# Kernel tuning notes

Hardware: AMD Instinct MI355X
Metric: run time of the kernel (lower is better)

Reference implementation:

```python
import jax, jax.numpy as jnp
import numpy as np

B, L, R, E, D = 16, 28, 64, 34, 512


def setup_inputs() -> dict:
    key = jax.random.key(0)
    ks = jax.random.split(key, 10)
    logits = jax.random.uniform(ks[0], (B, L, R), dtype=jnp.float32)
    evt_embeddings = jax.random.normal(ks[1], (B, 1, D), dtype=jnp.float32)
    arg_embeddings = jax.random.normal(ks[2], (B, L, D), dtype=jnp.float32)
    # valid-arg counts in [1, L] (used as mask-count multiplier and divisor)
    arg_padding_num = jax.random.randint(ks[3], (B,), 1, L + 1).astype(jnp.float32)
    evt_type_list = jax.random.randint(ks[4], (B,), 0, E)
    s = 1.0 / np.sqrt(D)
    WRT = jax.random.normal(ks[5], (R, D, D), dtype=jnp.float32) * s
    WTT = jax.random.normal(ks[6], (E, D, D), dtype=jnp.float32) * s
    w1 = jax.random.normal(ks[7], (D, 64), dtype=jnp.float32) * s
    b1 = jnp.zeros((64,), dtype=jnp.float32)
    w2 = jax.random.normal(ks[8], (64, 1), dtype=jnp.float32) * (1.0 / 8.0)
    b2 = jnp.zeros((1,), dtype=jnp.float32)
    return {"logits": logits, "evt_embeddings": evt_embeddings,
            "arg_embeddings": arg_embeddings, "arg_padding_num": arg_padding_num,
            "evt_type_list": evt_type_list, "WRT": WRT, "WTT": WTT,
            "w1": w1, "b1": b1, "w2": w2, "b2": b2}


def reference(logits, evt_embeddings, arg_embeddings, arg_padding_num,
              evt_type_list, WRT, WTT, w1, b1, w2, b2):
    # role transition matrix per (event, arg): one-hot/soft select over WRT
    # [B,L,R] x [R,D,D] -> [B,L,D,D]  (dominant, memory-bound intermediate)
    role_mats = jnp.einsum('blr,rde->blde', logits, WRT)
    # event transition matrix: one-hot select over WTT == gather
    evt_mats = WTT[evt_type_list]                      # [B,D,D]
    # event embedding transform: [B,1,D] bmm [B,D,D] -> [B,D]
    evt_trans = jnp.einsum('bd,bde->be', evt_embeddings[:, 0, :], evt_mats)
    # per-arg transform: [B,L,D] bmm [B,L,D,D] -> [B,L,D]
    role_trans = jnp.einsum('bld,blde->ble', arg_embeddings, role_mats)
    # multiply by count, sum over args, divide by count (as in the original)
    role_trans = role_trans * arg_padding_num[:, None, None]
    new_sum = jnp.sum(role_trans, axis=1)              # [B,D]
    div = new_sum / arg_padding_num[:, None]
    graph_embeddings = (div + evt_trans) / 2.0         # [B,D]
    # scorer MLP: Linear(D,64) -> ReLU -> Linear(64,1) -> Sigmoid
    h = jax.nn.relu(graph_embeddings @ w1 + b1)
    score = jax.nn.sigmoid(h @ w2 + b2)                # [B,1]
    return score
```

## Files before the change

kernel.cpp:

```cpp
#include <hip/hip_runtime.h>
#include <math.h>

#define BB 16
#define LL 28
#define RR 64
#define DD 512
#define NROLE 256
#define NEVT  256

__global__ void __launch_bounds__(256, 2) kernel_a(
    const float* __restrict__ logits,
    const float* __restrict__ arg,
    const float* __restrict__ WRT,
    const float* __restrict__ WTT,
    const float* __restrict__ evt_emb,
    const int*   __restrict__ evt_type,
    float* __restrict__ part,
    float* __restrict__ evt_part)
{
    __shared__ float smem[8192];
    const int t   = threadIdx.x;
    const int bid = blockIdx.x;

    if (bid < NROLE) {
        const int rid = bid;
        const int rp  = rid >> 3;
        const int d0  = (rid & 7) * 64;

        const float4* Wp0 = (const float4*)(WRT + ((size_t)(2 * rp)     * DD + d0) * DD);
        const float4* Wp1 = (const float4*)(WRT + ((size_t)(2 * rp + 1) * DD + d0) * DD);

        const int e4    = t & 127;
        const int h     = t >> 7;
        const int kbase = 32 * h;

        float4 w[8];
#pragma unroll
        for (int i = 0; i < 8; ++i)
            w[i] = Wp0[(size_t)(kbase + i) * 128 + e4];

        {
            const int b  = t >> 4;
            const int d4 = t & 15;
            const float4* ap = (const float4*)(arg) + (size_t)(b * LL) * 128 + (d0 >> 2) + d4;
            const float2* lp = (const float2*)(logits + (size_t)(b * LL) * RR) + rp;
            float4 g0 = {0.f, 0.f, 0.f, 0.f};
            float4 g1 = {0.f, 0.f, 0.f, 0.f};
#pragma unroll 7
            for (int l = 0; l < LL; ++l) {
                const float4 av = ap[(size_t)l * 128];
                const float2 lg = lp[(size_t)l * 32];
                g0.x = fmaf(lg.x, av.x, g0.x); g0.y = fmaf(lg.x, av.y, g0.y);
                g0.z = fmaf(lg.x, av.z, g0.z); g0.w = fmaf(lg.x, av.w, g0.w);
                g1.x = fmaf(lg.y, av.x, g1.x); g1.y = fmaf(lg.y, av.y, g1.y);
                g1.z = fmaf(lg.y, av.z, g1.z); g1.w = fmaf(lg.y, av.w, g1.w);
            }
            smem[(4 * d4 + 0) * 16 + b] = g0.x;
            smem[(4 * d4 + 1) * 16 + b] = g0.y;
            smem[(4 * d4 + 2) * 16 + b] = g0.z;
            smem[(4 * d4 + 3) * 16 + b] = g0.w;
            smem[1024 + (4 * d4 + 0) * 16 + b] = g1.x;
            smem[1024 + (4 * d4 + 1) * 16 + b] = g1.y;
            smem[1024 + (4 * d4 + 2) * 16 + b] = g1.z;
            smem[1024 + (4 * d4 + 3) * 16 + b] = g1.w;
        }
        __syncthreads();

        float4 acc[16];
#pragma unroll
        for (int i = 0; i < 16; ++i) acc[i] = make_float4(0.f, 0.f, 0.f, 0.f);

        for (int mb = 0; mb < 8; ++mb) {
            const int mbn = (mb + 1) & 7;
            const float4* Wn = (mbn & 4) ? Wp1 : Wp0;
            const int kn = kbase + (mbn & 3) * 8;
            float4 wn[8];
#pragma unroll
            for (int i = 0; i < 8; ++i)
                wn[i] = Wn[(size_t)(kn + i) * 128 + e4];

            const float* Gr = smem + (mb & 4) * 256;
            const int k0 = kbase + (mb & 3) * 8;
#pragma unroll
            for (int i = 0; i < 8; ++i) {
                const float* gp = Gr + (k0 + i) * 16;
                const float4 ga = ((const float4*)gp)[0];
                const float4 gb = ((const float4*)gp)[1];
                const float4 gc = ((const float4*)gp)[2];
                const float4 gd = ((const float4*)gp)[3];
#define ACC(j, S) \
                acc[j].x = fmaf(S, w[i].x, acc[j].x); \
                acc[j].y = fmaf(S, w[i].y, acc[j].y); \
                acc[j].z = fmaf(S, w[i].z, acc[j].z); \
                acc[j].w = fmaf(S, w[i].w, acc[j].w);
                ACC(0,  ga.x) ACC(1,  ga.y) ACC(2,  ga.z) ACC(3,  ga.w)
                ACC(4,  gb.x) ACC(5,  gb.y) ACC(6,  gb.z) ACC(7,  gb.w)
                ACC(8,  gc.x) ACC(9,  gc.y) ACC(10, gc.z) ACC(11, gc.w)
                ACC(12, gd.x) ACC(13, gd.y) ACC(14, gd.z) ACC(15, gd.w)
#undef ACC
            }
#pragma unroll
            for (int i = 0; i < 8; ++i) w[i] = wn[i];
        }

        __syncthreads();
        float4* cb = (float4*)smem;
        if (h == 1) {
#pragma unroll
            for (int i = 0; i < 16; ++i)
                cb[i * 128 + e4] = acc[i];
        }
        __syncthreads();
        if (h == 0) {
            float4* po = (float4*)part + (size_t)rid * 2048;
#pragma unroll
            for (int i = 0; i < 16; ++i) {
                const float4 v = cb[i * 128 + e4];
                acc[i].x += v.x; acc[i].y += v.y; acc[i].z += v.z; acc[i].w += v.w;
                po[i * 128 + e4] = acc[i];
            }
        }
    } else {
        const int cid = bid - NROLE;
        const int b   = cid >> 4;
        const int dc  = cid & 15;
        const int d0  = dc * 32;
        const int ty  = evt_type[b];
        const float* Wt = WTT + (size_t)ty * DD * DD;
        const int e4 = t & 127;
        const int s  = t >> 7;
        float4 a = {0.f, 0.f, 0.f, 0.f};
#pragma unroll
        for (int db = 0; db < 32; db += 16) {
            float  em[8];
            float4 wv[8];
#pragma unroll
            for (int i = 0; i < 8; ++i) {
                const int d = d0 + db + s + 2 * i;
                em[i] = evt_emb[b * DD + d];
                wv[i] = ((const float4*)(Wt + (size_t)d * DD))[e4];
            }
#pragma unroll
            for (int i = 0; i < 8; ++i) {
                a.x = fmaf(em[i], wv[i].x, a.x);
                a.y = fmaf(em[i], wv[i].y, a.y);
                a.z = fmaf(em[i], wv[i].z, a.z);
                a.w = fmaf(em[i], wv[i].w, a.w);
            }
        }
        float4* sm4 = (float4*)smem;
        if (s == 1) sm4[e4] = a;
        __syncthreads();
        if (s == 0) {
            const float4 q4 = sm4[e4];
            a.x += q4.x; a.y += q4.y; a.z += q4.z; a.w += q4.w;
            ((float4*)evt_part)[(size_t)cid * 128 + e4] = a;
        }
    }
}

__global__ void __launch_bounds__(256) kernel_reduce(
    const float* __restrict__ part,
    const float* __restrict__ evt_part,
    float* __restrict__ div_acc,
    float* __restrict__ evt_acc)
{
    const int t = threadIdx.x;
    if (blockIdx.x < 128) {
        __shared__ float4 sred[256];
        const int oo = t & 15;
        const int pg = t >> 4;
        const int o4 = blockIdx.x * 16 + oo;
        const float4* p4 = (const float4*)part;
        float4 s = {0.f, 0.f, 0.f, 0.f};
#pragma unroll 8
        for (int i = 0; i < 16; ++i) {
            const int p = pg * 16 + i;
            const float4 v = p4[(size_t)p * 2048 + o4];
            s.x += v.x; s.y += v.y; s.z += v.z; s.w += v.w;
        }
        sred[pg * 16 + oo] = s;
        __syncthreads();
        if (t < 16) {
            float4 tot = sred[t];
#pragma unroll
            for (int g = 1; g < 16; ++g) {
                const float4 v = sred[g * 16 + t];
                tot.x += v.x; tot.y += v.y; tot.z += v.z; tot.w += v.w;
            }
            ((float4*)div_acc)[blockIdx.x * 16 + t] = tot;
        }
    } else {
        const int o4 = (blockIdx.x - 128) * 256 + t;
        const int b  = o4 >> 7;
        const int el = o4 & 127;
        const float4* e4p = (const float4*)evt_part;
        float4 s = {0.f, 0.f, 0.f, 0.f};
#pragma unroll
        for (int dc = 0; dc < 16; ++dc) {
            const float4 v = e4p[(size_t)(b * 16 + dc) * 128 + el];
            s.x += v.x; s.y += v.y; s.z += v.z; s.w += v.w;
        }
        ((float4*)evt_acc)[o4] = s;
    }
}

__global__ void __launch_bounds__(256) kernel_mlp(
    const float* __restrict__ div_acc,
    const float* __restrict__ evt_acc,
    const float* __restrict__ w1,
    const float* __restrict__ b1,
    const float* __restrict__ w2,
    const float* __restrict__ b2,
    float* __restrict__ out)
{
    __shared__ float hred[256];
    const int b  = blockIdx.x;
    const int t  = threadIdx.x;
    const int j  = t & 63;
    const int dq = t >> 6;
    float hp = 0.f;
#pragma unroll 8
    for (int i = 0; i < 128; ++i) {
        const int d = dq * 128 + i;
        const float g = (div_acc[b * DD + d] + evt_acc[b * DD + d]) * 0.5f;
        hp = fmaf(g, w1[d * 64 + j], hp);
    }
    hred[t] = hp;
    __syncthreads();
    if (t < 64) {
        float h = b1[j] + hred[j] + hred[64 + j] + hred[128 + j] + hred[192 + j];
        h = fmaxf(h, 0.f);
        float v = h * w2[j];
#pragma unroll
        for (int off = 32; off > 0; off >>= 1) v += __shfl_down(v, off, 64);
        if (j == 0) out[b] = 1.f / (1.f + expf(-(v + b2[0])));
    }
}

extern "C" void kernel_launch(void* const* d_in, const int* in_sizes, int n_in,
                              void* d_out, int out_size, void* d_ws, size_t ws_size,
                              hipStream_t stream) {
    const float* logits   = (const float*)d_in[0];
    const float* evt_emb  = (const float*)d_in[1];
    const float* arg_emb  = (const float*)d_in[2];
    const int*   evt_type = (const int*)d_in[4];
    const float* WRT      = (const float*)d_in[5];
    const float* WTT      = (const float*)d_in[6];
    const float* w1       = (const float*)d_in[7];
    const float* b1       = (const float*)d_in[8];
    const float* w2       = (const float*)d_in[9];
    const float* b2       = (const float*)d_in[10];
    float* out = (float*)d_out;

    float* part     = (float*)d_ws;
    float* evt_part = part + (size_t)NROLE * 8192;
    float* div_acc  = evt_part + (size_t)NEVT * DD;
    float* evt_acc  = div_acc + BB * DD;

    hipLaunchKernelGGL(kernel_a, dim3(NROLE + NEVT), dim3(256), 0, stream,
                       logits, arg_emb, WRT, WTT, evt_emb, evt_type, part, evt_part);
    hipLaunchKernelGGL(kernel_reduce, dim3(136), dim3(256), 0, stream,
                       part, evt_part, div_acc, evt_acc);
    hipLaunchKernelGGL(kernel_mlp, dim3(BB), dim3(256), 0, stream,
                       div_acc, evt_acc, w1, b1, w2, b2, out);
}
```

Measured before the change: 152.1 us.

## Process four roles per block and fuse reduction with MLP tail kernel

Each role block now folds four role matrices (instead of two) into its accumulator, which halves the number of role blocks and the partial-sum traffic written to the workspace. The separate reduce and MLP kernels are merged into a single 1024-thread-per-batch tail kernel that reduces the partials, forms the graph embedding in shared memory, and runs the scorer. This removes one launch and a global round trip. In exchange there are fewer blocks to fill the GPU during the dominant WRT streaming phase, each block runs a longer serial loop, and the tail uses only 16 blocks.

```diff
diff --git a/kernel.cpp b/kernel.cpp
--- a/kernel.cpp
+++ b/kernel.cpp
@@ -5,8 +5,9 @@
 #define LL 28
 #define RR 64
 #define DD 512
-#define NROLE 256
+#define NROLE 128
 #define NEVT  256
+#define F4RR  65536
 
 __global__ void __launch_bounds__(256, 2) kernel_a(
     const float* __restrict__ logits,
@@ -27,8 +28,7 @@
         const int rp  = rid >> 3;
         const int d0  = (rid & 7) * 64;
 
-        const float4* Wp0 = (const float4*)(WRT + ((size_t)(2 * rp)     * DD + d0) * DD);
-        const float4* Wp1 = (const float4*)(WRT + ((size_t)(2 * rp + 1) * DD + d0) * DD);
+        const float4* WBase = (const float4*)(WRT + ((size_t)(4 * rp) * DD + d0) * DD);
 
         const int e4    = t & 127;
         const int h     = t >> 7;
@@ -37,32 +37,45 @@
         float4 w[8];
 #pragma unroll
         for (int i = 0; i < 8; ++i)
-            w[i] = Wp0[(size_t)(kbase + i) * 128 + e4];
+            w[i] = WBase[(size_t)(kbase + i) * 128 + e4];
 
         {
             const int b  = t >> 4;
             const int d4 = t & 15;
             const float4* ap = (const float4*)(arg) + (size_t)(b * LL) * 128 + (d0 >> 2) + d4;
-            const float2* lp = (const float2*)(logits + (size_t)(b * LL) * RR) + rp;
-            float4 g0 = {0.f, 0.f, 0.f, 0.f};
-            float4 g1 = {0.f, 0.f, 0.f, 0.f};
+            const float4* lp = (const float4*)(logits) + (size_t)(b * LL) * 16 + rp;
+            float4 g0 = {0.f,0.f,0.f,0.f}, g1 = {0.f,0.f,0.f,0.f};
+            float4 g2 = {0.f,0.f,0.f,0.f}, g3 = {0.f,0.f,0.f,0.f};
 #pragma unroll 7
             for (int l = 0; l < LL; ++l) {
                 const float4 av = ap[(size_t)l * 128];
-                const float2 lg = lp[(size_t)l * 32];
+                const float4 lg = lp[(size_t)l * 16];
                 g0.x = fmaf(lg.x, av.x, g0.x); g0.y = fmaf(lg.x, av.y, g0.y);
                 g0.z = fmaf(lg.x, av.z, g0.z); g0.w = fmaf(lg.x, av.w, g0.w);
                 g1.x = fmaf(lg.y, av.x, g1.x); g1.y = fmaf(lg.y, av.y, g1.y);
                 g1.z = fmaf(lg.y, av.z, g1.z); g1.w = fmaf(lg.y, av.w, g1.w);
-            }
-            smem[(4 * d4 + 0) * 16 + b] = g0.x;
-            smem[(4 * d4 + 1) * 16 + b] = g0.y;
-            smem[(4 * d4 + 2) * 16 + b] = g0.z;
-            smem[(4 * d4 + 3) * 16 + b] = g0.w;
-            smem[1024 + (4 * d4 + 0) * 16 + b] = g1.x;
-            smem[1024 + (4 * d4 + 1) * 16 + b] = g1.y;
-            smem[1024 + (4 * d4 + 2) * 16 + b] = g1.z;
-            smem[1024 + (4 * d4 + 3) * 16 + b] = g1.w;
+                g2.x = fmaf(lg.z, av.x, g2.x); g2.y = fmaf(lg.z, av.y, g2.y);
+                g2.z = fmaf(lg.z, av.z, g2.z); g2.w = fmaf(lg.z, av.w, g2.w);
+                g3.x = fmaf(lg.w, av.x, g3.x); g3.y = fmaf(lg.w, av.y, g3.y);
+                g3.z = fmaf(lg.w, av.z, g3.z); g3.w = fmaf(lg.w, av.w, g3.w);
+            }
+            const int row = 4 * d4;
+            smem[       (row + 0) * 16 + b] = g0.x;
+            smem[       (row + 1) * 16 + b] = g0.y;
+            smem[       (row + 2) * 16 + b] = g0.z;
+            smem[       (row + 3) * 16 + b] = g0.w;
+            smem[1024 + (row + 0) * 16 + b] = g1.x;
+            smem[1024 + (row + 1) * 16 + b] = g1.y;
+            smem[1024 + (row + 2) * 16 + b] = g1.z;
+            smem[1024 + (row + 3) * 16 + b] = g1.w;
+            smem[2048 + (row + 0) * 16 + b] = g2.x;
+            smem[2048 + (row + 1) * 16 + b] = g2.y;
+            smem[2048 + (row + 2) * 16 + b] = g2.z;
+            smem[2048 + (row + 3) * 16 + b] = g2.w;
+            smem[3072 + (row + 0) * 16 + b] = g3.x;
+            smem[3072 + (row + 1) * 16 + b] = g3.y;
+            smem[3072 + (row + 2) * 16 + b] = g3.z;
+            smem[3072 + (row + 3) * 16 + b] = g3.w;
         }
         __syncthreads();
 
@@ -70,16 +83,16 @@
 #pragma unroll
         for (int i = 0; i < 16; ++i) acc[i] = make_float4(0.f, 0.f, 0.f, 0.f);
 
-        for (int mb = 0; mb < 8; ++mb) {
-            const int mbn = (mb + 1) & 7;
-            const float4* Wn = (mbn & 4) ? Wp1 : Wp0;
+        for (int mb = 0; mb < 16; ++mb) {
+            const int mbn = (mb + 1) & 15;
+            const size_t nb = (size_t)(mbn >> 2) * F4RR;
             const int kn = kbase + (mbn & 3) * 8;
             float4 wn[8];
 #pragma unroll
             for (int i = 0; i < 8; ++i)
-                wn[i] = Wn[(size_t)(kn + i) * 128 + e4];
-
-            const float* Gr = smem + (mb & 4) * 256;
+                wn[i] = WBase[nb + (size_t)(kn + i) * 128 + e4];
+
+            const float* Gr = smem + (mb >> 2) * 1024;
             const int k0 = kbase + (mb & 3) * 8;
 #pragma unroll
             for (int i = 0; i < 8; ++i) {
@@ -159,82 +172,82 @@
     }
 }
 
-__global__ void __launch_bounds__(256) kernel_reduce(
+__global__ void __launch_bounds__(1024) kernel_tail(
     const float* __restrict__ part,
     const float* __restrict__ evt_part,
-    float* __restrict__ div_acc,
-    float* __restrict__ evt_acc)
-{
-    const int t = threadIdx.x;
-    if (blockIdx.x < 128) {
-        __shared__ float4 sred[256];
-        const int oo = t & 15;
-        const int pg = t >> 4;
-        const int o4 = blockIdx.x * 16 + oo;
-        const float4* p4 = (const float4*)part;
-        float4 s = {0.f, 0.f, 0.f, 0.f};
-#pragma unroll 8
-        for (int i = 0; i < 16; ++i) {
-            const int p = pg * 16 + i;
-            const float4 v = p4[(size_t)p * 2048 + o4];
-            s.x += v.x; s.y += v.y; s.z += v.z; s.w += v.w;
-        }
-        sred[pg * 16 + oo] = s;
-        __syncthreads();
-        if (t < 16) {
-            float4 tot = sred[t];
-#pragma unroll
-            for (int g = 1; g < 16; ++g) {
-                const float4 v = sred[g * 16 + t];
-                tot.x += v.x; tot.y += v.y; tot.z += v.z; tot.w += v.w;
-            }
-            ((float4*)div_acc)[blockIdx.x * 16 + t] = tot;
-        }
-    } else {
-        const int o4 = (blockIdx.x - 128) * 256 + t;
-        const int b  = o4 >> 7;
-        const int el = o4 & 127;
-        const float4* e4p = (const float4*)evt_part;
-        float4 s = {0.f, 0.f, 0.f, 0.f};
-#pragma unroll
-        for (int dc = 0; dc < 16; ++dc) {
-            const float4 v = e4p[(size_t)(b * 16 + dc) * 128 + el];
-            s.x += v.x; s.y += v.y; s.z += v.z; s.w += v.w;
-        }
-        ((float4*)evt_acc)[o4] = s;
-    }
-}
-
-__global__ void __launch_bounds__(256) kernel_mlp(
-    const float* __restrict__ div_acc,
-    const float* __restrict__ evt_acc,
     const float* __restrict__ w1,
     const float* __restrict__ b1,
     const float* __restrict__ w2,
     const float* __restrict__ b2,
     float* __restrict__ out)
 {
-    __shared__ float hred[256];
+    __shared__ float4 sm4[2048];
+    __shared__ float  gsm[512];
+    __shared__ float  hred[1024];
     const int b  = blockIdx.x;
     const int t  = threadIdx.x;
-    const int j  = t & 63;
-    const int dq = t >> 6;
-    float hp = 0.f;
+    const int e4 = t & 127;
+    const int g  = t >> 7;
+
+    const float4* p4  = (const float4*)part;
+    const float4* e4p = (const float4*)evt_part;
+    float4 s = {0.f, 0.f, 0.f, 0.f};
+#pragma unroll
+    for (int i = 0; i < 16; ++i) {
+        const int rid = g * 16 + i;
+        const float4 v = p4[(size_t)rid * 2048 + b * 128 + e4];
+        s.x += v.x; s.y += v.y; s.z += v.z; s.w += v.w;
+    }
+    sm4[g * 128 + e4] = s;
+    float4 es = {0.f, 0.f, 0.f, 0.f};
+#pragma unroll
+    for (int i = 0; i < 2; ++i) {
+        const int dc = g * 2 + i;
+        const float4 v = e4p[(size_t)(b * 16 + dc) * 128 + e4];
+        es.x += v.x; es.y += v.y; es.z += v.z; es.w += v.w;
+    }
+    sm4[1024 + g * 128 + e4] = es;
+    __syncthreads();
+
+    if (t < 128) {
+        float4 dv = {0.f,0.f,0.f,0.f}, ev = {0.f,0.f,0.f,0.f};
+#pragma unroll
+        for (int q = 0; q < 8; ++q) {
+            const float4 a = sm4[q * 128 + t];
+            const float4 c = sm4[1024 + q * 128 + t];
+            dv.x += a.x; dv.y += a.y; dv.z += a.z; dv.w += a.w;
+            ev.x += c.x; ev.y += c.y; ev.z += c.z; ev.w += c.w;
+        }
+        float4 gr;
+        gr.x = (dv.x + ev.x) * 0.5f;
+        gr.y = (dv.y + ev.y) * 0.5f;
+        gr.z = (dv.z + ev.z) * 0.5f;
+        gr.w = (dv.w + ev.w) * 0.5f;
+        ((float4*)gsm)[t] = gr;
+    }
+    __syncthreads();
+
+    {
+        const int j  = t & 63;
+        const int dq = t >> 6;
+        float hp = 0.f;
 #pragma unroll 8
-    for (int i = 0; i < 128; ++i) {
-        const int d = dq * 128 + i;
-        const float g = (div_acc[b * DD + d] + evt_acc[b * DD + d]) * 0.5f;
-        hp = fmaf(g, w1[d * 64 + j], hp);
-    }
-    hred[t] = hp;
+        for (int i = 0; i < 32; ++i) {
+            const int d = dq * 32 + i;
+            hp = fmaf(gsm[d], w1[d * 64 + j], hp);
+        }
+        hred[t] = hp;
+    }
     __syncthreads();
     if (t < 64) {
-        float h = b1[j] + hred[j] + hred[64 + j] + hred[128 + j] + hred[192 + j];
-        h = fmaxf(h, 0.f);
-        float v = h * w2[j];
+        float hh = b1[t];
+#pragma unroll
+        for (int q = 0; q < 16; ++q) hh += hred[q * 64 + t];
+        hh = fmaxf(hh, 0.f);
+        float v = hh * w2[t];
 #pragma unroll
         for (int off = 32; off > 0; off >>= 1) v += __shfl_down(v, off, 64);
-        if (j == 0) out[b] = 1.f / (1.f + expf(-(v + b2[0])));
+        if (t == 0) out[b] = 1.f / (1.f + expf(-(v + b2[0])));
     }
 }
 
@@ -255,13 +268,9 @@
 
     float* part     = (float*)d_ws;
     float* evt_part = part + (size_t)NROLE * 8192;
-    float* div_acc  = evt_part + (size_t)NEVT * DD;
-    float* evt_acc  = div_acc + BB * DD;
 
     hipLaunchKernelGGL(kernel_a, dim3(NROLE + NEVT), dim3(256), 0, stream,
                        logits, arg_emb, WRT, WTT, evt_emb, evt_type, part, evt_part);
-    hipLaunchKernelGGL(kernel_reduce, dim3(136), dim3(256), 0, stream,
-                       part, evt_part, div_acc, evt_acc);
-    hipLaunchKernelGGL(kernel_mlp, dim3(BB), dim3(256), 0, stream,
-                       div_acc, evt_acc, w1, b1, w2, b2, out);
+    hipLaunchKernelGGL(kernel_tail, dim3(BB), dim3(1024), 0, stream,
+                       part, evt_part, w1, b1, w2, b2, out);
 }
```

Result: slower. 157.0 us (+3.2%).
